# Kernel tuning notes

Hardware: AMD Instinct MI355X
Metric: run time of the kernel (lower is better)

The kernel has to match this reference:

```python
import jax, jax.numpy as jnp
import numpy as np

N_NODES = 100000
N_EDGES = 1600000
IN_C, HID_C, OUT_C = 128, 128, 64


def setup_inputs() -> dict:
    key = jax.random.key(0)
    ks = jax.random.split(key, 8)
    x = jax.random.normal(ks[0], (N_NODES, IN_C), dtype=jnp.float32)
    edge_index = jax.random.randint(ks[1], (2, N_EDGES), 0, N_NODES, dtype=jnp.int64)
    # SAGEConv params: lin_l (aggregated neighbors, with bias), lin_r (root, no bias)
    s1 = 1.0 / np.sqrt(IN_C)
    s2 = 1.0 / np.sqrt(HID_C)
    W1_l = jax.random.uniform(ks[2], (IN_C, HID_C), jnp.float32, -s1, s1)
    b1_l = jnp.zeros((HID_C,), jnp.float32)
    W1_r = jax.random.uniform(ks[3], (IN_C, HID_C), jnp.float32, -s1, s1)
    W2_l = jax.random.uniform(ks[4], (HID_C, OUT_C), jnp.float32, -s2, s2)
    b2_l = jnp.zeros((OUT_C,), jnp.float32)
    W2_r = jax.random.uniform(ks[5], (HID_C, OUT_C), jnp.float32, -s2, s2)
    return {"x": x, "edge_index": edge_index, "W1_l": W1_l, "b1_l": b1_l,
            "W1_r": W1_r, "W2_l": W2_l, "b2_l": b2_l, "W2_r": W2_r}


def _sage_conv(x, src, dst, W_l, b_l, W_r):
    # gather source features, scatter-max reduce onto destinations
    msg = x[src]                                             # [E, C]
    aggr = jax.ops.segment_max(msg, dst, num_segments=N_NODES)
    aggr = jnp.where(jnp.isfinite(aggr), aggr, 0.0)          # isolated nodes -> 0 (PyG behavior)
    return aggr @ W_l + b_l + x @ W_r


def reference(x, edge_index, W1_l, b1_l, W1_r, W2_l, b2_l, W2_r):
    src, dst = edge_index[0], edge_index[1]
    h = _sage_conv(x, src, dst, W1_l, b1_l, W1_r)
    h = jax.nn.relu(h)
    # dropout is identity in eval mode
    out = _sage_conv(h, src, dst, W2_l, b2_l, W2_r)
    return out
```

## Files before the change

### kernel.cpp

```cpp
#include <hip/hip_runtime.h>
#include <cstdint>

#define NNODES 100000
#define NEDGES 1600000
#define NBKT   196
#define CAP    9216
#define BIN_CHUNK 4096
#define GBIN ((NEDGES + BIN_CHUNK - 1) / BIN_CHUNK)
#define GCVT (NNODES * 128 / 8 / 256)

typedef __attribute__((ext_vector_type(8))) __bf16 bf16x8;
typedef __attribute__((ext_vector_type(4))) float f32x4;
typedef short v2s __attribute__((ext_vector_type(2)));

__device__ __forceinline__ unsigned short f2bf_rne(float f) {
    unsigned int u = __float_as_uint(f);
    u += 0x7fffu + ((u >> 16) & 1u);
    return (unsigned short)(u >> 16);
}
__device__ __forceinline__ unsigned encdec(unsigned u) {
    return u ^ (((u & 0x80008000u) >> 15) * 0x7FFFu);
}
__device__ __forceinline__ unsigned pkmax(unsigned a, unsigned b) {
    v2s r = __builtin_elementwise_max(__builtin_bit_cast(v2s, a), __builtin_bit_cast(v2s, b));
    return __builtin_bit_cast(unsigned, r);
}

__global__ __launch_bounds__(256) void prep1_kernel(
        const float* __restrict__ W1l, const float* __restrict__ W1r,
        const float* __restrict__ W2l, const float* __restrict__ W2r,
        uint4* __restrict__ Wf1, uint4* __restrict__ Wf2,
        int* __restrict__ bucketFill) {
    if (blockIdx.x == 24) { bucketFill[threadIdx.x] = 0; return; }
    int t = blockIdx.x * 256 + threadIdx.x;
    unsigned short s[8];
    if (t < 4096) {
        int h = t >> 11, kt = (t >> 9) & 3, nt = (t >> 6) & 7, lane = t & 63;
        const float* W = h ? W1r : W1l;
        int k0 = kt * 32 + (lane >> 4) * 8;
        int col = nt * 16 + (lane & 15);
#pragma unroll
        for (int j = 0; j < 8; ++j) s[j] = f2bf_rne(W[(k0 + j) * 128 + col]);
        uint4 o;
        o.x = (unsigned)s[0] | ((unsigned)s[1] << 16);
        o.y = (unsigned)s[2] | ((unsigned)s[3] << 16);
        o.z = (unsigned)s[4] | ((unsigned)s[5] << 16);
        o.w = (unsigned)s[6] | ((unsigned)s[7] << 16);
        Wf1[t] = o;
    } else {
        int u = t - 4096;
        int h = u >> 10, kt = (u >> 8) & 3, nt = (u >> 6) & 3, lane = u & 63;
        const float* W = h ? W2r : W2l;
        int k0 = kt * 32 + (lane >> 4) * 8;
        int col = nt * 16 + (lane & 15);
#pragma unroll
        for (int j = 0; j < 8; ++j) s[j] = f2bf_rne(W[(k0 + j) * 64 + col]);
        uint4 o;
        o.x = (unsigned)s[0] | ((unsigned)s[1] << 16);
        o.y = (unsigned)s[2] | ((unsigned)s[3] << 16);
        o.z = (unsigned)s[4] | ((unsigned)s[5] << 16);
        o.w = (unsigned)s[6] | ((unsigned)s[7] << 16);
        Wf2[u] = o;
    }
}

__global__ __launch_bounds__(256) void prep2_kernel(
        const int* __restrict__ src, const int* __restrict__ dst,
        unsigned int* __restrict__ binArr, int* __restrict__ bucketFill,
        const float4* __restrict__ xin, uint4* __restrict__ xeout, int nE) {
    if (blockIdx.x >= GBIN) {
        int i = (blockIdx.x - GBIN) * 256 + threadIdx.x;
        float4 v0 = xin[(size_t)2 * i], v1 = xin[(size_t)2 * i + 1];
        uint4 o;
        o.x = encdec((unsigned)f2bf_rne(v0.x) | ((unsigned)f2bf_rne(v0.y) << 16));
        o.y = encdec((unsigned)f2bf_rne(v0.z) | ((unsigned)f2bf_rne(v0.w) << 16));
        o.z = encdec((unsigned)f2bf_rne(v1.x) | ((unsigned)f2bf_rne(v1.y) << 16));
        o.w = encdec((unsigned)f2bf_rne(v1.z) | ((unsigned)f2bf_rne(v1.w) << 16));
        xeout[i] = o;
        return;
    }
    __shared__ unsigned int stage[BIN_CHUNK];
    __shared__ unsigned char bof[BIN_CHUNK];
    __shared__ int cnt[256], cstart[256], cfill[256], gbase[256];
    const int tid = threadIdx.x;
    const int blockStart = blockIdx.x * BIN_CHUNK;
    const int chunkN = min(BIN_CHUNK, nE - blockStart);
    cnt[tid] = 0;
    __syncthreads();
    int myd[16], mys[16];
#pragma unroll
    for (int i = 0; i < 16; ++i) {
        int idx = i * 256 + tid;
        if (idx < chunkN) {
            myd[i] = dst[blockStart + idx];
            mys[i] = src[blockStart + idx];
            atomicAdd(&cnt[myd[i] >> 9], 1);
        }
    }
    __syncthreads();
    int v = cnt[tid];
    for (int off = 1; off < 256; off <<= 1) {
        int add = (tid >= off) ? cnt[tid - off] : 0;
        __syncthreads();
        cnt[tid] += add;
        __syncthreads();
    }
    cstart[tid] = cnt[tid] - v;
    cfill[tid] = cnt[tid] - v;
    if (tid < NBKT && v > 0) gbase[tid] = atomicAdd(&bucketFill[tid], v);
    __syncthreads();
#pragma unroll
    for (int i = 0; i < 16; ++i) {
        int idx = i * 256 + tid;
        if (idx < chunkN) {
            int b = myd[i] >> 9;
            int p = atomicAdd(&cfill[b], 1);
            stage[p] = ((unsigned)(myd[i] & 511) << 17) | (unsigned)mys[i];
            bof[p] = (unsigned char)b;
        }
    }
    __syncthreads();
#pragma unroll
    for (int i = 0; i < 16; ++i) {
        int idx = i * 256 + tid;
        if (idx < chunkN) {
            int b = bof[idx];
            int slot = gbase[b] + (idx - cstart[b]);
            if (slot < CAP) binArr[(size_t)b * CAP + slot] = stage[idx];
        }
    }
}

__global__ __launch_bounds__(512) void build_csr_kernel(
        const unsigned int* __restrict__ binArr, const int* __restrict__ bucketFill,
        unsigned int* __restrict__ sortedSrc,
        int* __restrict__ rowBeg, int* __restrict__ rowEnd) {
    __shared__ unsigned int stage[CAP];
    __shared__ int ncnt[512], nstart[512];
    const int b = blockIdx.x;
    const int t = threadIdx.x;
    const int cnt_b = min(bucketFill[b], CAP);
    ncnt[t] = 0;
    __syncthreads();
    for (int i = t; i < cnt_b; i += 512) {
        unsigned int e = binArr[(size_t)b * CAP + i];
        stage[i] = e;
        atomicAdd(&ncnt[e >> 17], 1);
    }
    __syncthreads();
    int v = ncnt[t];
    for (int off = 1; off < 512; off <<= 1) {
        int add = (t >= off) ? ncnt[t - off] : 0;
        __syncthreads();
        ncnt[t] += add;
        __syncthreads();
    }
    int start = ncnt[t] - v;
    nstart[t] = start;
    int n = (b << 9) + t;
    if (n < NNODES) {
        rowBeg[n] = b * CAP + start;
        rowEnd[n] = b * CAP + start + v;
    }
    __syncthreads();
    for (int i = t; i < cnt_b; i += 512) {
        unsigned int e = stage[i];
        int p = atomicAdd(&nstart[e >> 17], 1);
        sortedSrc[(size_t)b * CAP + p] = e & 0x1FFFFu;
    }
}

template<int BN, bool RELU, bool ENCOUT, typename OutT>
__global__ __launch_bounds__(256, 6) void sage_fused(
        const uint4* __restrict__ xe4,
        const int* __restrict__ rowBeg,
        const int* __restrict__ rowEnd,
        const unsigned int* __restrict__ sortedSrc,
        const uint4* __restrict__ Wf,
        const float* __restrict__ bias,
        OutT* __restrict__ C,
        int M) {
    constexpr int NT = BN / 16;
    __shared__ __align__(16) unsigned short As[64 * 136];

    const int tid = threadIdx.x;
    const int w = tid >> 6;
    const int lane = tid & 63;
    const int grp = lane >> 4;
    const int c16 = lane & 15;
    const int base0 = blockIdx.x * 64;

    int bl = 0, el = 0;
    {
        int nn = base0 + w * 16 + c16;
        if (nn < M) { bl = rowBeg[nn]; el = rowEnd[nn]; }
    }
    int nbeg = __shfl(bl, 0), nend = __shfl(el, 0);
    int nid = (nend > nbeg) ? (int)sortedSrc[min(nbeg + lane, nend - 1)] : 0;
    for (int i = 0; i < 16; ++i) {
        const int beg = nbeg, end = nend;
        const int myid = nid;
        if (i < 15) {
            nbeg = __shfl(bl, i + 1);
            nend = __shfl(el, i + 1);
            nid = (nend > nbeg) ? (int)sortedSrc[min(nbeg + lane, nend - 1)] : 0;
        }
        const int r = w * 16 + i;
        if (end <= beg) {
            if (lane < 16) {
                uint4 z; z.x = z.y = z.z = z.w = 0u;
                ((uint4*)As)[r * 17 + c16] = z;
            }
            continue;
        }
        unsigned a0 = 0x80008000u, a1 = 0x80008000u, a2 = 0x80008000u, a3 = 0x80008000u;
        {
            const int m = min(end - beg, 64);
            for (int j = 0; j < m; j += 16) {
                int s0 = __shfl(myid, j + grp);
                int s1 = __shfl(myid, j + 4 + grp);
                int s2 = __shfl(myid, j + 8 + grp);
                int s3 = __shfl(myid, j + 12 + grp);
                uint4 p0 = xe4[(size_t)s0 * 16 + c16];
                uint4 p1 = xe4[(size_t)s1 * 16 + c16];
                uint4 p2 = xe4[(size_t)s2 * 16 + c16];
                uint4 p3 = xe4[(size_t)s3 * 16 + c16];
                a0 = pkmax(a0, pkmax(pkmax(p0.x, p1.x), pkmax(p2.x, p3.x)));
                a1 = pkmax(a1, pkmax(pkmax(p0.y, p1.y), pkmax(p2.y, p3.y)));
                a2 = pkmax(a2, pkmax(pkmax(p0.z, p1.z), pkmax(p2.z, p3.z)));
                a3 = pkmax(a3, pkmax(pkmax(p0.w, p1.w), pkmax(p2.w, p3.w)));
            }
        }
        for (int bs = beg + 64; bs < end; bs += 64) {
            int bid = (int)sortedSrc[min(bs + lane, end - 1)];
            const int m = min(end - bs, 64);
            for (int j = 0; j < m; j += 16) {
                int s0 = __shfl(bid, j + grp);
                int s1 = __shfl(bid, j + 4 + grp);
                int s2 = __shfl(bid, j + 8 + grp);
                int s3 = __shfl(bid, j + 12 + grp);
                uint4 p0 = xe4[(size_t)s0 * 16 + c16];
                uint4 p1 = xe4[(size_t)s1 * 16 + c16];
                uint4 p2 = xe4[(size_t)s2 * 16 + c16];
                uint4 p3 = xe4[(size_t)s3 * 16 + c16];
                a0 = pkmax(a0, pkmax(pkmax(p0.x, p1.x), pkmax(p2.x, p3.x)));
                a1 = pkmax(a1, pkmax(pkmax(p0.y, p1.y), pkmax(p2.y, p3.y)));
                a2 = pkmax(a2, pkmax(pkmax(p0.z, p1.z), pkmax(p2.z, p3.z)));
                a3 = pkmax(a3, pkmax(pkmax(p0.w, p1.w), pkmax(p2.w, p3.w)));
            }
        }
        a0 = pkmax(a0, (unsigned)__shfl_xor((int)a0, 16));
        a1 = pkmax(a1, (unsigned)__shfl_xor((int)a1, 16));
        a2 = pkmax(a2, (unsigned)__shfl_xor((int)a2, 16));
        a3 = pkmax(a3, (unsigned)__shfl_xor((int)a3, 16));
        a0 = pkmax(a0, (unsigned)__shfl_xor((int)a0, 32));
        a1 = pkmax(a1, (unsigned)__shfl_xor((int)a1, 32));
        a2 = pkmax(a2, (unsigned)__shfl_xor((int)a2, 32));
        a3 = pkmax(a3, (unsigned)__shfl_xor((int)a3, 32));
        if (lane < 16) {
            uint4 o;
            o.x = encdec(a0); o.y = encdec(a1); o.z = encdec(a2); o.w = encdec(a3);
            ((uint4*)As)[r * 17 + c16] = o;
        }
    }

    f32x4 acc[NT];
#pragma unroll
    for (int nt = 0; nt < NT; ++nt) acc[nt] = (f32x4){0.f, 0.f, 0.f, 0.f};

    const int rowR = base0 + w * 16 + c16;
    const int rowRc = (rowR < M) ? rowR : 0;
#pragma unroll
    for (int kt = 0; kt < 4; ++kt) {
        bf16x8 aa = *(const bf16x8*)(As + (w * 16 + c16) * 136 + kt * 32 + grp * 8);
        uint4 tr = xe4[(size_t)rowRc * 16 + kt * 4 + grp];
        tr.x = encdec(tr.x); tr.y = encdec(tr.y); tr.z = encdec(tr.z); tr.w = encdec(tr.w);
        bf16x8 ar = __builtin_bit_cast(bf16x8, tr);
#pragma unroll
        for (int nt = 0; nt < NT; ++nt) {
            bf16x8 b0 = __builtin_bit_cast(bf16x8, Wf[(kt * NT + nt) * 64 + lane]);
            acc[nt] = __builtin_amdgcn_mfma_f32_16x16x32_bf16(aa, b0, acc[nt], 0, 0, 0);
            bf16x8 b1 = __builtin_bit_cast(bf16x8, Wf[((4 + kt) * NT + nt) * 64 + lane]);
            acc[nt] = __builtin_amdgcn_mfma_f32_16x16x32_bf16(ar, b1, acc[nt], 0, 0, 0);
        }
    }

    const int rowD = base0 + w * 16 + grp * 4;
#pragma unroll
    for (int nt = 0; nt < NT; ++nt) {
        int col = nt * 16 + c16;
        float bv = bias[col];
#pragma unroll
        for (int r = 0; r < 4; ++r) {
            int grow = rowD + r;
            if (grow < M) {
                float v = acc[nt][r] + bv;
                if (RELU) v = fmaxf(v, 0.0f);
                if constexpr (ENCOUT) {
                    unsigned u = f2bf_rne(v);
                    u ^= ((u >> 15) & 1u) * 0x7FFFu;
                    C[(size_t)grow * BN + col] = (OutT)u;
                } else {
                    C[(size_t)grow * BN + col] = (OutT)v;
                }
            }
        }
    }
}

extern "C" void kernel_launch(void* const* d_in, const int* in_sizes, int n_in,
                              void* d_out, int out_size, void* d_ws, size_t ws_size,
                              hipStream_t stream) {
    const float* x   = (const float*)d_in[0];
    const int*   ei  = (const int*)d_in[1];
    const float* W1l = (const float*)d_in[2];
    const float* b1l = (const float*)d_in[3];
    const float* W1r = (const float*)d_in[4];
    const float* W2l = (const float*)d_in[5];
    const float* b2l = (const float*)d_in[6];
    const float* W2r = (const float*)d_in[7];
    float* out = (float*)d_out;

    const int* src = ei;
    const int* dst = ei + NEDGES;

    char* ws = (char*)d_ws;
    unsigned short* xe = (unsigned short*)ws; ws += (size_t)NNODES * 128 * 2;
    unsigned short* he = (unsigned short*)ws; ws += (size_t)NNODES * 128 * 2;
    unsigned int* binArr    = (unsigned int*)ws; ws += (size_t)NBKT * CAP * 4;
    unsigned int* sortedSrc = (unsigned int*)ws; ws += (size_t)NBKT * CAP * 4;
    int* rowBeg     = (int*)ws; ws += (size_t)NNODES * 4;
    int* rowEnd     = (int*)ws; ws += (size_t)NNODES * 4;
    int* bucketFill = (int*)ws; ws += 256 * 4;
    uint4* Wf1 = (uint4*)ws; ws += 4096 * 16;
    uint4* Wf2 = (uint4*)ws; ws += 2048 * 16;

    const int gGemm = (NNODES + 63) / 64;

    prep1_kernel<<<25, 256, 0, stream>>>(W1l, W1r, W2l, W2r, Wf1, Wf2, bucketFill);
    prep2_kernel<<<GBIN + GCVT, 256, 0, stream>>>(src, dst, binArr, bucketFill,
                                                  (const float4*)x, (uint4*)xe, NEDGES);
    build_csr_kernel<<<NBKT, 512, 0, stream>>>(binArr, bucketFill, sortedSrc, rowBeg, rowEnd);

    sage_fused<128, true, true, unsigned short><<<gGemm, 256, 0, stream>>>(
        (const uint4*)xe, rowBeg, rowEnd, sortedSrc, Wf1, b1l, he, NNODES);
    sage_fused<64, false, false, float><<<gGemm, 256, 0, stream>>>(
        (const uint4*)he, rowBeg, rowEnd, sortedSrc, Wf2, b2l, out, NNODES);
}
```

Baseline: 297.9 us.

## Split fused gather-max+GEMM into separate aggregate and GEMM kernels

```diff
diff --git a/kernel.cpp b/kernel.cpp
--- a/kernel.cpp
+++ b/kernel.cpp
@@ -170,138 +170,203 @@
     }
 }
 
-template<int BN, bool RELU, bool ENCOUT, typename OutT>
-__global__ __launch_bounds__(256, 6) void sage_fused(
+__global__ __launch_bounds__(256) void aggregate_pk2(
         const uint4* __restrict__ xe4,
         const int* __restrict__ rowBeg,
         const int* __restrict__ rowEnd,
         const unsigned int* __restrict__ sortedSrc,
+        uint4* __restrict__ aggrE,
+        int nN) {
+    const int wv = threadIdx.x >> 6;
+    const int lane = threadIdx.x & 63;
+    const int grp = lane >> 4;
+    const int nA = blockIdx.x * 8 + wv * 2;
+    const int nB = nA + 1;
+    if (nA >= nN) return;
+    const int begA = rowBeg[nA], endA = rowEnd[nA];
+    int begB = 0, endB = 0;
+    if (nB < nN) { begB = rowBeg[nB]; endB = rowEnd[nB]; }
+    const int mA = endA - begA, mB = endB - begB;
+
+    int idA = (mA > 0) ? (int)sortedSrc[min(begA + lane, endA - 1)] : 0;
+    int idB = (mB > 0) ? (int)sortedSrc[min(begB + lane, endB - 1)] : 0;
+
+    unsigned aA0 = 0x80008000u, aA1 = 0x80008000u, aA2 = 0x80008000u, aA3 = 0x80008000u;
+    unsigned aB0 = 0x80008000u, aB1 = 0x80008000u, aB2 = 0x80008000u, aB3 = 0x80008000u;
+
+    const int cA = min(mA, 64), cB = min(mB, 64);
+    const int mm = max(cA, cB);
+    for (int j = 0; j < mm; j += 16) {
+        const bool doA = j < cA, doB = j < cB;
+        uint4 pA0, pA1, pA2, pA3, pB0, pB1, pB2, pB3;
+        if (doA) {
+            int s0 = __shfl(idA, j + grp);
+            int s1 = __shfl(idA, j + 4 + grp);
+            int s2 = __shfl(idA, j + 8 + grp);
+            int s3 = __shfl(idA, j + 12 + grp);
+            pA0 = xe4[(size_t)s0 * 16 + (lane & 15)];
+            pA1 = xe4[(size_t)s1 * 16 + (lane & 15)];
+            pA2 = xe4[(size_t)s2 * 16 + (lane & 15)];
+            pA3 = xe4[(size_t)s3 * 16 + (lane & 15)];
+        }
+        if (doB) {
+            int s0 = __shfl(idB, j + grp);
+            int s1 = __shfl(idB, j + 4 + grp);
+            int s2 = __shfl(idB, j + 8 + grp);
+            int s3 = __shfl(idB, j + 12 + grp);
+            pB0 = xe4[(size_t)s0 * 16 + (lane & 15)];
+            pB1 = xe4[(size_t)s1 * 16 + (lane & 15)];
+            pB2 = xe4[(size_t)s2 * 16 + (lane & 15)];
+            pB3 = xe4[(size_t)s3 * 16 + (lane & 15)];
+        }
+        if (doA) {
+            aA0 = pkmax(aA0, pkmax(pkmax(pA0.x, pA1.x), pkmax(pA2.x, pA3.x)));
+            aA1 = pkmax(aA1, pkmax(pkmax(pA0.y, pA1.y), pkmax(pA2.y, pA3.y)));
+            aA2 = pkmax(aA2, pkmax(pkmax(pA0.z, pA1.z), pkmax(pA2.z, pA3.z)));
+            aA3 = pkmax(aA3, pkmax(pkmax(pA0.w, pA1.w), pkmax(pA2.w, pA3.w)));
+        }
+        if (doB) {
+            aB0 = pkmax(aB0, pkmax(pkmax(pB0.x, pB1.x), pkmax(pB2.x, pB3.x)));
+            aB1 = pkmax(aB1, pkmax(pkmax(pB0.y, pB1.y), pkmax(pB2.y, pB3.y)));
+            aB2 = pkmax(aB2, pkmax(pkmax(pB0.z, pB1.z), pkmax(pB2.z, pB3.z)));
+            aB3 = pkmax(aB3, pkmax(pkmax(pB0.w, pB1.w), pkmax(pB2.w, pB3.w)));
+        }
+    }
+    for (int bs = begA + 64; bs < endA; bs += 64) {
+        int bid = (int)sortedSrc[min(bs + lane, endA - 1)];
+        const int m = min(endA - bs, 64);
+        for (int j = 0; j < m; j += 16) {
+            int s0 = __shfl(bid, j + grp);
+            int s1 = __shfl(bid, j + 4 + grp);
+            int s2 = __shfl(bid, j + 8 + grp);
+            int s3 = __shfl(bid, j + 12 + grp);
+            uint4 p0 = xe4[(size_t)s0 * 16 + (lane & 15)];
+            uint4 p1 = xe4[(size_t)s1 * 16 + (lane & 15)];
+            uint4 p2 = xe4[(size_t)s2 * 16 + (lane & 15)];
+            uint4 p3 = xe4[(size_t)s3 * 16 + (lane & 15)];
+            aA0 = pkmax(aA0, pkmax(pkmax(p0.x, p1.x), pkmax(p2.x, p3.x)));
+            aA1 = pkmax(aA1, pkmax(pkmax(p0.y, p1.y), pkmax(p2.y, p3.y)));
+            aA2 = pkmax(aA2, pkmax(pkmax(p0.z, p1.z), pkmax(p2.z, p3.z)));
+            aA3 = pkmax(aA3, pkmax(pkmax(p0.w, p1.w), pkmax(p2.w, p3.w)));
+        }
+    }
+    for (int bs = begB + 64; bs < endB; bs += 64) {
+        int bid = (int)sortedSrc[min(bs + lane, endB - 1)];
+        const int m = min(endB - bs, 64);
+        for (int j = 0; j < m; j += 16) {
+            int s0 = __shfl(bid, j + grp);
+            int s1 = __shfl(bid, j + 4 + grp);
+            int s2 = __shfl(bid, j + 8 + grp);
+            int s3 = __shfl(bid, j + 12 + grp);
+            uint4 p0 = xe4[(size_t)s0 * 16 + (lane & 15)];
+            uint4 p1 = xe4[(size_t)s1 * 16 + (lane & 15)];
+            uint4 p2 = xe4[(size_t)s2 * 16 + (lane & 15)];
+            uint4 p3 = xe4[(size_t)s3 * 16 + (lane & 15)];
+            aB0 = pkmax(aB0, pkmax(pkmax(p0.x, p1.x), pkmax(p2.x, p3.x)));
+            aB1 = pkmax(aB1, pkmax(pkmax(p0.y, p1.y), pkmax(p2.y, p3.y)));
+            aB2 = pkmax(aB2, pkmax(pkmax(p0.z, p1.z), pkmax(p2.z, p3.z)));
+            aB3 = pkmax(aB3, pkmax(pkmax(p0.w, p1.w), pkmax(p2.w, p3.w)));
+        }
+    }
+    aA0 = pkmax(aA0, (unsigned)__shfl_xor((int)aA0, 16));
+    aA1 = pkmax(aA1, (unsigned)__shfl_xor((int)aA1, 16));
+    aA2 = pkmax(aA2, (unsigned)__shfl_xor((int)aA2, 16));
+    aA3 = pkmax(aA3, (unsigned)__shfl_xor((int)aA3, 16));
+    aB0 = pkmax(aB0, (unsigned)__shfl_xor((int)aB0, 16));
+    aB1 = pkmax(aB1, (unsigned)__shfl_xor((int)aB1, 16));
+    aB2 = pkmax(aB2, (unsigned)__shfl_xor((int)aB2, 16));
+    aB3 = pkmax(aB3, (unsigned)__shfl_xor((int)aB3, 16));
+    aA0 = pkmax(aA0, (unsigned)__shfl_xor((int)aA0, 32));
+    aA1 = pkmax(aA1, (unsigned)__shfl_xor((int)aA1, 32));
+    aA2 = pkmax(aA2, (unsigned)__shfl_xor((int)aA2, 32));
+    aA3 = pkmax(aA3, (unsigned)__shfl_xor((int)aA3, 32));
+    aB0 = pkmax(aB0, (unsigned)__shfl_xor((int)aB0, 32));
+    aB1 = pkmax(aB1, (unsigned)__shfl_xor((int)aB1, 32));
+    aB2 = pkmax(aB2, (unsigned)__shfl_xor((int)aB2, 32));
+    aB3 = pkmax(aB3, (unsigned)__shfl_xor((int)aB3, 32));
+    if (lane < 16) {
+        uint4 o;
+        if (mA > 0) { o.x = aA0; o.y = aA1; o.z = aA2; o.w = aA3; }
+        else        { o.x = o.y = o.z = o.w = 0u; }
+        aggrE[(size_t)nA * 16 + lane] = o;
+    } else if (lane < 32 && nB < nN) {
+        uint4 o;
+        if (mB > 0) { o.x = aB0; o.y = aB1; o.z = aB2; o.w = aB3; }
+        else        { o.x = o.y = o.z = o.w = 0u; }
+        aggrE[(size_t)nB * 16 + (lane - 16)] = o;
+    }
+}
+
+template<int BN, bool RELU, bool ENCOUT, typename OutT>
+__global__ __launch_bounds__(256, 4) void sage_gemm_lean(
+        const uint4* __restrict__ AggE,
+        const uint4* __restrict__ RootE,
         const uint4* __restrict__ Wf,
         const float* __restrict__ bias,
         OutT* __restrict__ C,
         int M) {
     constexpr int NT = BN / 16;
-    __shared__ __align__(16) unsigned short As[64 * 136];
-
     const int tid = threadIdx.x;
     const int w = tid >> 6;
     const int lane = tid & 63;
-    const int grp = lane >> 4;
-    const int c16 = lane & 15;
-    const int base0 = blockIdx.x * 64;
-
-    int bl = 0, el = 0;
-    {
-        int nn = base0 + w * 16 + c16;
-        if (nn < M) { bl = rowBeg[nn]; el = rowEnd[nn]; }
-    }
-    int nbeg = __shfl(bl, 0), nend = __shfl(el, 0);
-    int nid = (nend > nbeg) ? (int)sortedSrc[min(nbeg + lane, nend - 1)] : 0;
-    for (int i = 0; i < 16; ++i) {
-        const int beg = nbeg, end = nend;
-        const int myid = nid;
-        if (i < 15) {
-            nbeg = __shfl(bl, i + 1);
-            nend = __shfl(el, i + 1);
-            nid = (nend > nbeg) ? (int)sortedSrc[min(nbeg + lane, nend - 1)] : 0;
-        }
-        const int r = w * 16 + i;
-        if (end <= beg) {
-            if (lane < 16) {
-                uint4 z; z.x = z.y = z.z = z.w = 0u;
-                ((uint4*)As)[r * 17 + c16] = z;
-            }
-            continue;
-        }
-        unsigned a0 = 0x80008000u, a1 = 0x80008000u, a2 = 0x80008000u, a3 = 0x80008000u;
-        {
-            const int m = min(end - beg, 64);
-            for (int j = 0; j < m; j += 16) {
-                int s0 = __shfl(myid, j + grp);
-                int s1 = __shfl(myid, j + 4 + grp);
-                int s2 = __shfl(myid, j + 8 + grp);
-                int s3 = __shfl(myid, j + 12 + grp);
-                uint4 p0 = xe4[(size_t)s0 * 16 + c16];
-                uint4 p1 = xe4[(size_t)s1 * 16 + c16];
-                uint4 p2 = xe4[(size_t)s2 * 16 + c16];
-                uint4 p3 = xe4[(size_t)s3 * 16 + c16];
-                a0 = pkmax(a0, pkmax(pkmax(p0.x, p1.x), pkmax(p2.x, p3.x)));
-                a1 = pkmax(a1, pkmax(pkmax(p0.y, p1.y), pkmax(p2.y, p3.y)));
-                a2 = pkmax(a2, pkmax(pkmax(p0.z, p1.z), pkmax(p2.z, p3.z)));
-                a3 = pkmax(a3, pkmax(pkmax(p0.w, p1.w), pkmax(p2.w, p3.w)));
-            }
-        }
-        for (int bs = beg + 64; bs < end; bs += 64) {
-            int bid = (int)sortedSrc[min(bs + lane, end - 1)];
-            const int m = min(end - bs, 64);
-            for (int j = 0; j < m; j += 16) {
-                int s0 = __shfl(bid, j + grp);
-                int s1 = __shfl(bid, j + 4 + grp);
-                int s2 = __shfl(bid, j + 8 + grp);
-                int s3 = __shfl(bid, j + 12 + grp);
-                uint4 p0 = xe4[(size_t)s0 * 16 + c16];
-                uint4 p1 = xe4[(size_t)s1 * 16 + c16];
-                uint4 p2 = xe4[(size_t)s2 * 16 + c16];
-                uint4 p3 = xe4[(size_t)s3 * 16 + c16];
-                a0 = pkmax(a0, pkmax(pkmax(p0.x, p1.x), pkmax(p2.x, p3.x)));
-                a1 = pkmax(a1, pkmax(pkmax(p0.y, p1.y), pkmax(p2.y, p3.y)));
-                a2 = pkmax(a2, pkmax(pkmax(p0.z, p1.z), pkmax(p2.z, p3.z)));
-                a3 = pkmax(a3, pkmax(pkmax(p0.w, p1.w), pkmax(p2.w, p3.w)));
-            }
-        }
-        a0 = pkmax(a0, (unsigned)__shfl_xor((int)a0, 16));
-        a1 = pkmax(a1, (unsigned)__shfl_xor((int)a1, 16));
-        a2 = pkmax(a2, (unsigned)__shfl_xor((int)a2, 16));
-        a3 = pkmax(a3, (unsigned)__shfl_xor((int)a3, 16));
-        a0 = pkmax(a0, (unsigned)__shfl_xor((int)a0, 32));
-        a1 = pkmax(a1, (unsigned)__shfl_xor((int)a1, 32));
-        a2 = pkmax(a2, (unsigned)__shfl_xor((int)a2, 32));
-        a3 = pkmax(a3, (unsigned)__shfl_xor((int)a3, 32));
-        if (lane < 16) {
-            uint4 o;
-            o.x = encdec(a0); o.y = encdec(a1); o.z = encdec(a2); o.w = encdec(a3);
-            ((uint4*)As)[r * 17 + c16] = o;
-        }
-    }
-
-    f32x4 acc[NT];
-#pragma unroll
-    for (int nt = 0; nt < NT; ++nt) acc[nt] = (f32x4){0.f, 0.f, 0.f, 0.f};
-
-    const int rowR = base0 + w * 16 + c16;
-    const int rowRc = (rowR < M) ? rowR : 0;
+    const int quad = lane >> 4;
+    const int mrow = lane & 15;
+    const int base0 = blockIdx.x * 128 + w * 32;
+
+    const int r0 = min(base0 + mrow, M - 1);
+    const int r1 = min(base0 + 16 + mrow, M - 1);
+
+    f32x4 acc[2][NT];
+#pragma unroll
+    for (int mt = 0; mt < 2; ++mt)
+#pragma unroll
+        for (int nt = 0; nt < NT; ++nt) acc[mt][nt] = (f32x4){0.f, 0.f, 0.f, 0.f};
+
 #pragma unroll
     for (int kt = 0; kt < 4; ++kt) {
-        bf16x8 aa = *(const bf16x8*)(As + (w * 16 + c16) * 136 + kt * 32 + grp * 8);
-        uint4 tr = xe4[(size_t)rowRc * 16 + kt * 4 + grp];
-        tr.x = encdec(tr.x); tr.y = encdec(tr.y); tr.z = encdec(tr.z); tr.w = encdec(tr.w);
-        bf16x8 ar = __builtin_bit_cast(bf16x8, tr);
+        uint4 ta0 = AggE[(size_t)r0 * 16 + kt * 4 + quad];
+        uint4 ta1 = AggE[(size_t)r1 * 16 + kt * 4 + quad];
+        uint4 tr0 = RootE[(size_t)r0 * 16 + kt * 4 + quad];
+        uint4 tr1 = RootE[(size_t)r1 * 16 + kt * 4 + quad];
+        ta0.x = encdec(ta0.x); ta0.y = encdec(ta0.y); ta0.z = encdec(ta0.z); ta0.w = encdec(ta0.w);
+        ta1.x = encdec(ta1.x); ta1.y = encdec(ta1.y); ta1.z = encdec(ta1.z); ta1.w = encdec(ta1.w);
+        tr0.x = encdec(tr0.x); tr0.y = encdec(tr0.y); tr0.z = encdec(tr0.z); tr0.w = encdec(tr0.w);
+        tr1.x = encdec(tr1.x); tr1.y = encdec(tr1.y); tr1.z = encdec(tr1.z); tr1.w = encdec(tr1.w);
+        bf16x8 aa0 = __builtin_bit_cast(bf16x8, ta0);
+        bf16x8 aa1 = __builtin_bit_cast(bf16x8, ta1);
+        bf16x8 ar0 = __builtin_bit_cast(bf16x8, tr0);
+        bf16x8 ar1 = __builtin_bit_cast(bf16x8, tr1);
 #pragma unroll
         for (int nt = 0; nt < NT; ++nt) {
             bf16x8 b0 = __builtin_bit_cast(bf16x8, Wf[(kt * NT + nt) * 64 + lane]);
-            acc[nt] = __builtin_amdgcn_mfma_f32_16x16x32_bf16(aa, b0, acc[nt], 0, 0, 0);
+            acc[0][nt] = __builtin_amdgcn_mfma_f32_16x16x32_bf16(aa0, b0, acc[0][nt], 0, 0, 0);
+            acc[1][nt] = __builtin_amdgcn_mfma_f32_16x16x32_bf16(aa1, b0, acc[1][nt], 0, 0, 0);
             bf16x8 b1 = __builtin_bit_cast(bf16x8, Wf[((4 + kt) * NT + nt) * 64 + lane]);
-            acc[nt] = __builtin_amdgcn_mfma_f32_16x16x32_bf16(ar, b1, acc[nt], 0, 0, 0);
-        }
-    }
-
-    const int rowD = base0 + w * 16 + grp * 4;
-#pragma unroll
-    for (int nt = 0; nt < NT; ++nt) {
-        int col = nt * 16 + c16;
-        float bv = bias[col];
-#pragma unroll
-        for (int r = 0; r < 4; ++r) {
-            int grow = rowD + r;
-            if (grow < M) {
-                float v = acc[nt][r] + bv;
-                if (RELU) v = fmaxf(v, 0.0f);
-                if constexpr (ENCOUT) {
-                    unsigned u = f2bf_rne(v);
-                    u ^= ((u >> 15) & 1u) * 0x7FFFu;
-                    C[(size_t)grow * BN + col] = (OutT)u;
-                } else {
-                    C[(size_t)grow * BN + col] = (OutT)v;
+            acc[0][nt] = __builtin_amdgcn_mfma_f32_16x16x32_bf16(ar0, b1, acc[0][nt], 0, 0, 0);
+            acc[1][nt] = __builtin_amdgcn_mfma_f32_16x16x32_bf16(ar1, b1, acc[1][nt], 0, 0, 0);
+        }
+    }
+
+#pragma unroll
+    for (int mt = 0; mt < 2; ++mt) {
+        const int rowD = base0 + mt * 16 + quad * 4;
+#pragma unroll
+        for (int nt = 0; nt < NT; ++nt) {
+            int col = nt * 16 + mrow;
+            float bv = bias[col];
+#pragma unroll
+            for (int r = 0; r < 4; ++r) {
+                int grow = rowD + r;
+                if (grow < M) {
+                    float v = acc[mt][nt][r] + bv;
+                    if (RELU) v = fmaxf(v, 0.0f);
+                    if constexpr (ENCOUT) {
+                        unsigned u = f2bf_rne(v);
+                        u ^= ((u >> 15) & 1u) * 0x7FFFu;
+                        C[(size_t)grow * BN + col] = (OutT)u;
+                    } else {
+                        C[(size_t)grow * BN + col] = (OutT)v;
+                    }
                 }
             }
         }
@@ -325,8 +390,9 @@
     const int* dst = ei + NEDGES;
 
     char* ws = (char*)d_ws;
-    unsigned short* xe = (unsigned short*)ws; ws += (size_t)NNODES * 128 * 2;
-    unsigned short* he = (unsigned short*)ws; ws += (size_t)NNODES * 128 * 2;
+    unsigned short* xe    = (unsigned short*)ws; ws += (size_t)NNODES * 128 * 2;
+    unsigned short* he    = (unsigned short*)ws; ws += (size_t)NNODES * 128 * 2;
+    unsigned short* aggrE = (unsigned short*)ws; ws += (size_t)NNODES * 128 * 2;
     unsigned int* binArr    = (unsigned int*)ws; ws += (size_t)NBKT * CAP * 4;
     unsigned int* sortedSrc = (unsigned int*)ws; ws += (size_t)NBKT * CAP * 4;
     int* rowBeg     = (int*)ws; ws += (size_t)NNODES * 4;
@@ -335,15 +401,20 @@
     uint4* Wf1 = (uint4*)ws; ws += 4096 * 16;
     uint4* Wf2 = (uint4*)ws; ws += 2048 * 16;
 
-    const int gGemm = (NNODES + 63) / 64;
+    const int gAgg = (NNODES + 7) / 8;
+    const int gGemm = (NNODES + 127) / 128;
 
     prep1_kernel<<<25, 256, 0, stream>>>(W1l, W1r, W2l, W2r, Wf1, Wf2, bucketFill);
     prep2_kernel<<<GBIN + GCVT, 256, 0, stream>>>(src, dst, binArr, bucketFill,
                                                   (const float4*)x, (uint4*)xe, NEDGES);
     build_csr_kernel<<<NBKT, 512, 0, stream>>>(binArr, bucketFill, sortedSrc, rowBeg, rowEnd);
 
-    sage_fused<128, true, true, unsigned short><<<gGemm, 256, 0, stream>>>(
-        (const uint4*)xe, rowBeg, rowEnd, sortedSrc, Wf1, b1l, he, NNODES);
-    sage_fused<64, false, false, float><<<gGemm, 256, 0, stream>>>(
-        (const uint4*)he, rowBeg, rowEnd, sortedSrc, Wf2, b2l, out, NNODES);
-}
+    aggregate_pk2<<<gAgg, 256, 0, stream>>>((const uint4*)xe, rowBeg, rowEnd, sortedSrc,
+                                            (uint4*)aggrE, NNODES);
+    sage_gemm_lean<128, true, true, unsigned short><<<gGemm, 256, 0, stream>>>(
+        (const uint4*)aggrE, (const uint4*)xe, Wf1, b1l, he, NNODES);
+    aggregate_pk2<<<gAgg, 256, 0, stream>>>((const uint4*)he, rowBeg, rowEnd, sortedSrc,
+                                            (uint4*)aggrE, NNODES);
+    sage_gemm_lean<64, false, false, float><<<gGemm, 256, 0, stream>>>(
+        (const uint4*)aggrE, (const uint4*)he, Wf2, b2l, out, NNODES);
+}
```

After: 294.2 us. About the same (-1.3%).
